# Kernel optimization log

Measured on AMD Instinct MI355X. Metric: run time of the kernel, lower is better.

## Reference

```python
import jax, jax.numpy as jnp
import numpy as np

T, B, I, H = 100, 64, 256, 512


def setup_inputs() -> dict:
    key = jax.random.key(0)
    ks = jax.random.split(key, 7)
    # torch kaiming_uniform_(a=sqrt(5)) + fan_in bias init -> uniform(-1/sqrt(fan_in), 1/sqrt(fan_in))
    b_ih = 1.0 / np.sqrt(I)
    b_hh = 1.0 / np.sqrt(H)
    return {
        "input": jax.random.normal(ks[0], (T, B, I), jnp.float32),
        "initial_h": jax.random.normal(ks[1], (B, H), jnp.float32),
        "initial_c": jax.random.normal(ks[2], (B, H), jnp.float32),
        "weight_ih": jax.random.uniform(ks[3], (4 * H, I), jnp.float32, -b_ih, b_ih),
        "weight_hh": jax.random.uniform(ks[4], (4 * H, H), jnp.float32, -b_hh, b_hh),
        "bias_ih": jax.random.uniform(ks[5], (4 * H,), jnp.float32, -b_ih, b_ih),
        "bias_hh": jax.random.uniform(ks[6], (4 * H,), jnp.float32, -b_hh, b_hh),
    }


def reference(input, initial_h, initial_c, weight_ih, weight_hh, bias_ih, bias_hh):
    Bsz, Isz = input.shape[1], input.shape[2]
    Hs = initial_h.shape[1]

    def step(carry, x_t):
        hx, cx, ev_ih, ev_hh, ev_b = carry
        # standard LSTM gates, torch gate order: i, f, g, o
        gates = x_t @ weight_ih.T + hx @ weight_hh.T + bias_ih + bias_hh  # [B,4H]
        i_g, f_g, g_g, o_g = jnp.split(gates, 4, axis=1)
        i = jax.nn.sigmoid(i_g)
        f = jax.nn.sigmoid(f_g)
        g = jnp.tanh(g_g)
        o = jax.nn.sigmoid(o_g)
        cy = f * cx + i * g
        hy = o * jnp.tanh(cy)
        # e-prop instantaneous derivatives of c_t wrt the i/f/g pre-activations
        d_i = g * i * (1.0 - i)          # [B,H]
        d_f = cx * f * (1.0 - f)
        d_g = i * (1.0 - g * g)
        d = jnp.concatenate([d_i, d_f, d_g], axis=1)[:, :, None]  # [B,3H,1]
        f3 = jnp.tile(f, (1, 3))[:, :, None]                      # [B,3H,1]
        # eligibility-trace recursion: ev_t = f_t * ev_{t-1} + d_t (outer) input
        ev_ih = f3 * ev_ih + d * x_t[:, None, :]   # [B,3H,I]
        ev_hh = f3 * ev_hh + d * hx[:, None, :]    # [B,3H,H]
        ev_b = f3 * ev_b + d                       # [B,3H,1]
        return (hy, cy, ev_ih, ev_hh, ev_b), hy

    ev_ih0 = jnp.zeros((Bsz, 3 * Hs, Isz), input.dtype)
    ev_hh0 = jnp.zeros((Bsz, 3 * Hs, Hs), input.dtype)
    ev_b0 = jnp.zeros((Bsz, 3 * Hs, 1), input.dtype)
    (hx, cx, ev_ih, ev_hh, ev_b), outputs = jax.lax.scan(
        step, (initial_h, initial_c, ev_ih0, ev_hh0, ev_b0), input
    )
    return outputs, cx, ev_ih, ev_hh, ev_b
```

## Files before the change

kernel.cpp:

```cpp
#include <hip/hip_runtime.h>
#include <math.h>

#define TT 100
#define BB 64
#define II 256
#define HH 512
#define G4H 2048
#define G3H 1536
#define NBLK 256

#define OFF_GT    0
#define OFF_HBUF  13107200
#define OFF_FBUF  16416768
#define OFF_DBUF  19693568
#define OFF_CT    29523968
#define OFF_XT    29556736
#define OFF_WIHT  31195136
#define OFF_WHHT  31719424

#define O_OUT   0
#define O_CX    3276800
#define O_EVIH  3309568
#define O_EVHH  28475392
#define O_EVB   78807040

__global__ __launch_bounds__(256) void tp64(const float* __restrict__ src,
                                            float* __restrict__ dst,
                                            int R, int C,
                                            long sstride, long dstride) {
  __shared__ float tile[64][65];
  src += (long)blockIdx.z * sstride;
  dst += (long)blockIdx.z * dstride;
  int r0 = blockIdx.y * 64, c0 = blockIdx.x * 64;
  int tx = threadIdx.x & 15, tq = threadIdx.x >> 4;
#pragma unroll
  for (int p = 0; p < 4; ++p) {
    int rl = p * 16 + tq;
    float4 v = *(const float4*)(src + (long)(r0 + rl) * C + c0 + tx * 4);
    tile[rl][tx * 4 + 0] = v.x; tile[rl][tx * 4 + 1] = v.y;
    tile[rl][tx * 4 + 2] = v.z; tile[rl][tx * 4 + 3] = v.w;
  }
  __syncthreads();
#pragma unroll
  for (int p = 0; p < 4; ++p) {
    int cl = p * 16 + tq;
    float4 v;
    v.x = tile[tx * 4 + 0][cl]; v.y = tile[tx * 4 + 1][cl];
    v.z = tile[tx * 4 + 2][cl]; v.w = tile[tx * 4 + 3][cl];
    *(float4*)(dst + (long)(c0 + cl) * R + r0 + tx * 4) = v;
  }
}

__global__ __launch_bounds__(256) void make_whhg(const float* __restrict__ WhhT,
                                                 float* __restrict__ WhhG,
                                                 int* __restrict__ bar) {
  int gid = blockIdx.x * 256 + threadIdx.x;
  if (gid < NBLK) bar[gid] = 0;
  int k = gid >> 11, j = gid & 2047;
  float v = WhhT[gid];
  WhhG[(long)k * G4H + ((j & 511) << 2) + (j >> 9)] = v;
}

template <int BK, int KTILES, bool BIAS, bool ZSHIFT>
__global__ __launch_bounds__(256) void gemm_tn(
    const float* __restrict__ A, long batchA, int lda,
    const float* __restrict__ Z, long batchZ, int ldz,
    const float* __restrict__ Z0, long batchZ0,
    float* __restrict__ C, long batchC, int ldc,
    const float* __restrict__ bia, const float* __restrict__ bib) {
  __shared__ float As[BK][64];
  __shared__ float Zs[BK][64];
  int tid = threadIdx.x;
  int tn = tid & 15, tm = tid >> 4;
  int m0 = blockIdx.x * 64, n0 = blockIdx.y * 64;
  long bz = blockIdx.z;
  const float* Ab = A + bz * batchA + m0;
  const float* Zb = Z + bz * batchZ + n0;
  const float* Z0b = ZSHIFT ? (Z0 + bz * batchZ0 + n0) : nullptr;
  float acc[4][4] = {};
  for (int kt = 0; kt < KTILES; ++kt) {
    int k0 = kt * BK;
#pragma unroll
    for (int p = tid; p < BK * 64; p += 256) {
      int r = p >> 6, c = p & 63;
      int k = k0 + r;
      As[r][c] = Ab[(long)k * lda + c];
      const float* zr;
      if (ZSHIFT)
        zr = (k == 0) ? Z0b : (Zb + (long)(k - 1) * ldz);
      else
        zr = Zb + (long)k * ldz;
      Zs[r][c] = zr[c];
    }
    __syncthreads();
#pragma unroll 4
    for (int kk = 0; kk < BK; ++kk) {
      float4 a = *(const float4*)&As[kk][tm * 4];
      float4 z = *(const float4*)&Zs[kk][tn * 4];
      float av[4] = {a.x, a.y, a.z, a.w};
      float zv[4] = {z.x, z.y, z.z, z.w};
#pragma unroll
      for (int q = 0; q < 4; ++q)
#pragma unroll
        for (int r = 0; r < 4; ++r)
          acc[q][r] = fmaf(av[q], zv[r], acc[q][r]);
    }
    __syncthreads();
  }
  float* Cb = C + bz * batchC + n0 + tn * 4;
#pragma unroll
  for (int q = 0; q < 4; ++q) {
    int m = m0 + tm * 4 + q;
    float bv = BIAS ? (bia[m] + bib[m]) : 0.f;
    float4 v;
    v.x = acc[q][0] + bv; v.y = acc[q][1] + bv;
    v.z = acc[q][2] + bv; v.w = acc[q][3] + bv;
    *(float4*)(Cb + (long)m * ldc) = v;
  }
}

__global__ __launch_bounds__(512) void lstm_rec(
    const float* __restrict__ G_T, const float* __restrict__ WhhG,
    float* __restrict__ Hbuf, float* __restrict__ cT,
    float* __restrict__ Fbuf, float* __restrict__ Dbuf,
    int* __restrict__ bar) {
  __shared__ float red[8][8][64];
  int tid = threadIdx.x;
  int lane = tid & 63;
  int wave = __builtin_amdgcn_readfirstlane(tid >> 6);
  int bx = blockIdx.x;
  const float* wp = WhhG + (long)(wave * 64) * G4H + bx * 8;
  int h2 = tid >> 6;
  int b = tid & 63;
  float creg = 0.f;
  if (tid < 128) creg = cT[(bx * 2 + h2) * BB + b];

  float gpre0 = 0.f, gpre1 = 0.f, gpre2 = 0.f, gpre3 = 0.f;
  if (tid < 128) {
    const float* gp = G_T + (bx * 2 + h2) * BB + b;
    gpre0 = gp[0l * HH * BB];
    gpre1 = gp[1l * HH * BB];
    gpre2 = gp[2l * HH * BB];
    gpre3 = gp[3l * HH * BB];
  }

  int myflag = wave * 32 + (lane & 31);

  for (int t = 0; t < TT; ++t) {
    const float* hp = Hbuf + (long)t * (HH * BB) + (wave * 64) * BB + lane;
    float hv[64];
#pragma unroll
    for (int k = 0; k < 64; ++k) hv[k] = hp[(long)k * BB];
    float a0 = 0.f, a1 = 0.f, a2 = 0.f, a3 = 0.f;
    float a4 = 0.f, a5 = 0.f, a6 = 0.f, a7 = 0.f;
#pragma unroll
    for (int k = 0; k < 64; ++k) {
      float h = hv[k];
      float4 w0 = *(const float4*)(wp + (long)k * G4H);
      float4 w1 = *(const float4*)(wp + (long)k * G4H + 4);
      a0 = fmaf(w0.x, h, a0); a1 = fmaf(w0.y, h, a1);
      a2 = fmaf(w0.z, h, a2); a3 = fmaf(w0.w, h, a3);
      a4 = fmaf(w1.x, h, a4); a5 = fmaf(w1.y, h, a5);
      a6 = fmaf(w1.z, h, a6); a7 = fmaf(w1.w, h, a7);
    }
    red[wave][0][lane] = a0; red[wave][1][lane] = a1;
    red[wave][2][lane] = a2; red[wave][3][lane] = a3;
    red[wave][4][lane] = a4; red[wave][5][lane] = a5;
    red[wave][6][lane] = a6; red[wave][7][lane] = a7;
    __syncthreads();
    if (tid < 128) {
      float g0 = gpre0, g1 = gpre1, g2 = gpre2, g3 = gpre3;
#pragma unroll
      for (int kp = 0; kp < 8; ++kp) {
        g0 += red[kp][h2 * 4 + 0][b];
        g1 += red[kp][h2 * 4 + 1][b];
        g2 += red[kp][h2 * 4 + 2][b];
        g3 += red[kp][h2 * 4 + 3][b];
      }
      float ig = 1.f / (1.f + expf(-g0));
      float fg = 1.f / (1.f + expf(-g1));
      float gg = tanhf(g2);
      float og = 1.f / (1.f + expf(-g3));
      int idx = (bx * 2 + h2) * BB + b;
      float co = creg;
      float cy = fg * co + ig * gg;
      creg = cy;
      __hip_atomic_store(&Hbuf[(long)(t + 1) * (HH * BB) + idx],
                         og * tanhf(cy), __ATOMIC_RELAXED,
                         __HIP_MEMORY_SCOPE_AGENT);
      Fbuf[(long)t * (HH * BB) + idx] = fg;
      float* dp = Dbuf + (long)t * (G3H * BB) + idx;
      dp[0] = gg * ig * (1.f - ig);
      dp[HH * BB] = co * fg * (1.f - fg);
      dp[2 * HH * BB] = ig * (1.f - gg * gg);
    }
    __syncthreads();
    if (t < TT - 1) {
      if (tid == 0)
        __hip_atomic_store(&bar[bx], t + 1, __ATOMIC_RELAXED,
                           __HIP_MEMORY_SCOPE_AGENT);
      if (tid < 128) {
        const float* gp =
            G_T + (long)(t + 1) * (G4H * BB) + (bx * 2 + h2) * BB + b;
        gpre0 = gp[0l * HH * BB];
        gpre1 = gp[1l * HH * BB];
        gpre2 = gp[2l * HH * BB];
        gpre3 = gp[3l * HH * BB];
      }
      {
        int tgt = t + 1;
        while (true) {
          int v = __hip_atomic_load(&bar[myflag], __ATOMIC_RELAXED,
                                    __HIP_MEMORY_SCOPE_AGENT);
          if (__all(v >= tgt)) break;
          __builtin_amdgcn_s_sleep(1);
        }
      }
      asm volatile("" ::: "memory");
    }
  }
  if (tid < 128) cT[(bx * 2 + h2) * BB + b] = creg;
}

__global__ __launch_bounds__(256) void suffix_scale(float* __restrict__ Dbuf,
                                                    const float* __restrict__ Fbuf,
                                                    float* __restrict__ evb) {
  int g = blockIdx.x * 256 + threadIdx.x;
  int b = g & 63, hh = g >> 6;
  float P = 1.f, e0 = 0.f, e1 = 0.f, e2 = 0.f;
#pragma unroll 2
  for (int t = TT - 1; t >= 0; --t) {
    float* dp = Dbuf + (long)t * (G3H * BB) + hh * BB + b;
    float v0 = dp[0] * P, v1 = dp[HH * BB] * P, v2 = dp[2 * HH * BB] * P;
    dp[0] = v0; dp[HH * BB] = v1; dp[2 * HH * BB] = v2;
    e0 += v0; e1 += v1; e2 += v2;
    P *= Fbuf[(long)t * (HH * BB) + hh * BB + b];
  }
  evb[b * G3H + hh] = e0;
  evb[b * G3H + HH + hh] = e1;
  evb[b * G3H + 2 * HH + hh] = e2;
}

extern "C" void kernel_launch(void* const* d_in, const int* in_sizes, int n_in,
                              void* d_out, int out_size, void* d_ws, size_t ws_size,
                              hipStream_t stream) {
  const float* x   = (const float*)d_in[0];
  const float* h0  = (const float*)d_in[1];
  const float* c0  = (const float*)d_in[2];
  const float* Wih = (const float*)d_in[3];
  const float* Whh = (const float*)d_in[4];
  const float* bih = (const float*)d_in[5];
  const float* bhh = (const float*)d_in[6];
  float* out = (float*)d_out;
  float* ws = (float*)d_ws;

  float* G_T   = ws + OFF_GT;
  float* DbufT = ws + OFF_GT;
  float* Hbuf  = ws + OFF_HBUF;
  float* Fbuf  = ws + OFF_FBUF;
  float* Dbuf  = ws + OFF_DBUF;
  float* cT    = ws + OFF_CT;
  float* xT    = ws + OFF_XT;
  float* WhhG  = ws + OFF_XT;
  float* WihT  = ws + OFF_WIHT;
  int*   bar   = (int*)(ws + OFF_WIHT);
  float* WhhT  = ws + OFF_WHHT;

  tp64<<<dim3(II / 64, G4H / 64, 1), 256, 0, stream>>>(Wih, WihT, G4H, II, 0, 0);
  tp64<<<dim3(HH / 64, G4H / 64, 1), 256, 0, stream>>>(Whh, WhhT, G4H, HH, 0, 0);
  tp64<<<dim3(II / 64, 1, TT), 256, 0, stream>>>(x, xT, BB, II, BB * II, BB * II);
  tp64<<<dim3(HH / 64, 1, 1), 256, 0, stream>>>(h0, Hbuf, BB, HH, 0, 0);
  tp64<<<dim3(HH / 64, 1, 1), 256, 0, stream>>>(c0, cT, BB, HH, 0, 0);

  gemm_tn<64, 4, true, false><<<dim3(G4H / 64, 1, TT), 256, 0, stream>>>(
      WihT, 0, G4H, xT, (long)II * BB, BB, nullptr, 0,
      G_T, (long)G4H * BB, BB, bih, bhh);

  make_whhg<<<dim3(HH * G4H / 256, 1, 1), 256, 0, stream>>>(WhhT, WhhG, bar);

  {
    const float* a_gt = G_T;
    const float* a_wg = WhhG;
    float* a_hb = Hbuf;
    float* a_ct = cT;
    float* a_fb = Fbuf;
    float* a_db = Dbuf;
    int* a_bar = bar;
    void* args[] = {(void*)&a_gt, (void*)&a_wg, (void*)&a_hb, (void*)&a_ct,
                    (void*)&a_fb, (void*)&a_db, (void*)&a_bar};
    hipLaunchCooperativeKernel((const void*)lstm_rec, dim3(NBLK), dim3(512),
                               args, 0, stream);
  }

  suffix_scale<<<dim3(HH * BB / 256, 1, 1), 256, 0, stream>>>(Dbuf, Fbuf,
                                                              out + O_EVB);

  tp64<<<dim3(1, TT * G3H / 64, 1), 256, 0, stream>>>(Dbuf, DbufT, TT * G3H, BB,
                                                      0, 0);

  tp64<<<dim3(1, HH / 64, TT), 256, 0, stream>>>(Hbuf + HH * BB, out + O_OUT,
                                                 HH, BB, HH * BB, HH * BB);
  tp64<<<dim3(1, HH / 64, 1), 256, 0, stream>>>(cT, out + O_CX, HH, BB, 0, 0);

  gemm_tn<20, 5, false, false><<<dim3(G3H / 64, II / 64, BB), 256, 0, stream>>>(
      DbufT, (long)TT * G3H, G3H, x, (long)II, (long)BB * II, nullptr, 0,
      out + O_EVIH, (long)G3H * II, II, nullptr, nullptr);

  gemm_tn<20, 5, false, true><<<dim3(G3H / 64, HH / 64, BB), 256, 0, stream>>>(
      DbufT, (long)TT * G3H, G3H, out + O_OUT, (long)HH, (long)BB * HH,
      h0, (long)HH,
      out + O_EVHH, (long)G3H * HH, HH, nullptr, nullptr);
}
```

Before: 1.568 ms.

## Cache recurrent weights in LDS and pipeline gate waves with per-column flags

Each block of the recurrent LSTM kernel now loads its slice of the recurrent weight matrix into LDS once, instead of re-reading it from global memory every timestep. The block grows to ten waves: eight compute the matvec and two dedicated waves apply the gate nonlinearities one step behind, using a double-buffered reduction array. The single per-block barrier flag is replaced by per-column-pair flags, published after a waitcnt by the gate waves. Consumers spin only on the flags they need, which shortens the global synchronization critical path at the cost of more flag polling and larger blocks.

```diff
diff --git a/kernel.cpp b/kernel.cpp
--- a/kernel.cpp
+++ b/kernel.cpp
@@ -55,7 +55,7 @@
                                                  float* __restrict__ WhhG,
                                                  int* __restrict__ bar) {
   int gid = blockIdx.x * 256 + threadIdx.x;
-  if (gid < NBLK) bar[gid] = 0;
+  if (gid < 2 * NBLK) bar[gid] = 0;
   int k = gid >> 11, j = gid & 2047;
   float v = WhhT[gid];
   WhhG[(long)k * G4H + ((j & 511) << 2) + (j >> 9)] = v;
@@ -119,63 +119,84 @@
   }
 }
 
-__global__ __launch_bounds__(512) void lstm_rec(
+__global__ __launch_bounds__(640) void lstm_rec(
     const float* __restrict__ G_T, const float* __restrict__ WhhG,
     float* __restrict__ Hbuf, float* __restrict__ cT,
     float* __restrict__ Fbuf, float* __restrict__ Dbuf,
     int* __restrict__ bar) {
-  __shared__ float red[8][8][64];
+  __shared__ float lds_w[4096];
+  __shared__ float red[2][8][8][64];
   int tid = threadIdx.x;
   int lane = tid & 63;
   int wave = __builtin_amdgcn_readfirstlane(tid >> 6);
   int bx = blockIdx.x;
-  const float* wp = WhhG + (long)(wave * 64) * G4H + bx * 8;
-  int h2 = tid >> 6;
-  int b = tid & 63;
+
+  {
+    float4* d4 = (float4*)lds_w;
+    const float4* s4 = (const float4*)WhhG;
+    for (int n = tid; n < 1024; n += 640) {
+      int k = n >> 1, half = n & 1;
+      d4[n] = s4[(long)k * 512 + bx * 2 + half];
+    }
+  }
+
+  int h2 = wave - 8;
+  int b = lane;
   float creg = 0.f;
-  if (tid < 128) creg = cT[(bx * 2 + h2) * BB + b];
-
   float gpre0 = 0.f, gpre1 = 0.f, gpre2 = 0.f, gpre3 = 0.f;
-  if (tid < 128) {
+  if (wave >= 8) {
+    creg = cT[(bx * 2 + h2) * BB + b];
     const float* gp = G_T + (bx * 2 + h2) * BB + b;
     gpre0 = gp[0l * HH * BB];
     gpre1 = gp[1l * HH * BB];
     gpre2 = gp[2l * HH * BB];
     gpre3 = gp[3l * HH * BB];
   }
-
-  int myflag = wave * 32 + (lane & 31);
+  __syncthreads();
 
   for (int t = 0; t < TT; ++t) {
-    const float* hp = Hbuf + (long)t * (HH * BB) + (wave * 64) * BB + lane;
-    float hv[64];
-#pragma unroll
-    for (int k = 0; k < 64; ++k) hv[k] = hp[(long)k * BB];
-    float a0 = 0.f, a1 = 0.f, a2 = 0.f, a3 = 0.f;
-    float a4 = 0.f, a5 = 0.f, a6 = 0.f, a7 = 0.f;
-#pragma unroll
-    for (int k = 0; k < 64; ++k) {
-      float h = hv[k];
-      float4 w0 = *(const float4*)(wp + (long)k * G4H);
-      float4 w1 = *(const float4*)(wp + (long)k * G4H + 4);
-      a0 = fmaf(w0.x, h, a0); a1 = fmaf(w0.y, h, a1);
-      a2 = fmaf(w0.z, h, a2); a3 = fmaf(w0.w, h, a3);
-      a4 = fmaf(w1.x, h, a4); a5 = fmaf(w1.y, h, a5);
-      a6 = fmaf(w1.z, h, a6); a7 = fmaf(w1.w, h, a7);
-    }
-    red[wave][0][lane] = a0; red[wave][1][lane] = a1;
-    red[wave][2][lane] = a2; red[wave][3][lane] = a3;
-    red[wave][4][lane] = a4; red[wave][5][lane] = a5;
-    red[wave][6][lane] = a6; red[wave][7][lane] = a7;
-    __syncthreads();
-    if (tid < 128) {
+    if (wave < 8) {
+      if (t > 0) {
+        int myflag = wave * 64 + lane;
+        while (true) {
+          int v = __hip_atomic_load(&bar[myflag], __ATOMIC_RELAXED,
+                                    __HIP_MEMORY_SCOPE_AGENT);
+          if (__all(v >= t)) break;
+          __builtin_amdgcn_s_sleep(1);
+        }
+        asm volatile("" ::: "memory");
+      }
+      const float* hp = Hbuf + (long)t * (HH * BB) + (wave * 64) * BB + lane;
+      float hv[64];
+#pragma unroll
+      for (int k = 0; k < 64; ++k) hv[k] = hp[(long)k * BB];
+      float a0 = 0.f, a1 = 0.f, a2 = 0.f, a3 = 0.f;
+      float a4 = 0.f, a5 = 0.f, a6 = 0.f, a7 = 0.f;
+      const float4* w4 = (const float4*)lds_w + wave * 128;
+#pragma unroll
+      for (int k = 0; k < 64; ++k) {
+        float4 w0 = w4[2 * k];
+        float4 w1 = w4[2 * k + 1];
+        float h = hv[k];
+        a0 = fmaf(w0.x, h, a0); a1 = fmaf(w0.y, h, a1);
+        a2 = fmaf(w0.z, h, a2); a3 = fmaf(w0.w, h, a3);
+        a4 = fmaf(w1.x, h, a4); a5 = fmaf(w1.y, h, a5);
+        a6 = fmaf(w1.z, h, a6); a7 = fmaf(w1.w, h, a7);
+      }
+      int p = t & 1;
+      red[p][wave][0][lane] = a0; red[p][wave][1][lane] = a1;
+      red[p][wave][2][lane] = a2; red[p][wave][3][lane] = a3;
+      red[p][wave][4][lane] = a4; red[p][wave][5][lane] = a5;
+      red[p][wave][6][lane] = a6; red[p][wave][7][lane] = a7;
+    } else if (t > 0) {
+      int p = (t - 1) & 1;
       float g0 = gpre0, g1 = gpre1, g2 = gpre2, g3 = gpre3;
 #pragma unroll
       for (int kp = 0; kp < 8; ++kp) {
-        g0 += red[kp][h2 * 4 + 0][b];
-        g1 += red[kp][h2 * 4 + 1][b];
-        g2 += red[kp][h2 * 4 + 2][b];
-        g3 += red[kp][h2 * 4 + 3][b];
+        g0 += red[p][kp][h2 * 4 + 0][b];
+        g1 += red[p][kp][h2 * 4 + 1][b];
+        g2 += red[p][kp][h2 * 4 + 2][b];
+        g3 += red[p][kp][h2 * 4 + 3][b];
       }
       float ig = 1.f / (1.f + expf(-g0));
       float fg = 1.f / (1.f + expf(-g1));
@@ -185,41 +206,51 @@
       float co = creg;
       float cy = fg * co + ig * gg;
       creg = cy;
-      __hip_atomic_store(&Hbuf[(long)(t + 1) * (HH * BB) + idx],
-                         og * tanhf(cy), __ATOMIC_RELAXED,
-                         __HIP_MEMORY_SCOPE_AGENT);
-      Fbuf[(long)t * (HH * BB) + idx] = fg;
-      float* dp = Dbuf + (long)t * (G3H * BB) + idx;
+      __hip_atomic_store(&Hbuf[(long)t * (HH * BB) + idx], og * tanhf(cy),
+                         __ATOMIC_RELAXED, __HIP_MEMORY_SCOPE_AGENT);
+      Fbuf[(long)(t - 1) * (HH * BB) + idx] = fg;
+      float* dp = Dbuf + (long)(t - 1) * (G3H * BB) + idx;
       dp[0] = gg * ig * (1.f - ig);
       dp[HH * BB] = co * fg * (1.f - fg);
       dp[2 * HH * BB] = ig * (1.f - gg * gg);
+      asm volatile("s_waitcnt vmcnt(0)" ::: "memory");
+      if (lane == 0)
+        __hip_atomic_store(&bar[bx * 2 + h2], t, __ATOMIC_RELAXED,
+                           __HIP_MEMORY_SCOPE_AGENT);
+      const float* gp = G_T + (long)t * (G4H * BB) + (bx * 2 + h2) * BB + b;
+      gpre0 = gp[0l * HH * BB];
+      gpre1 = gp[1l * HH * BB];
+      gpre2 = gp[2l * HH * BB];
+      gpre3 = gp[3l * HH * BB];
     }
     __syncthreads();
-    if (t < TT - 1) {
-      if (tid == 0)
-        __hip_atomic_store(&bar[bx], t + 1, __ATOMIC_RELAXED,
-                           __HIP_MEMORY_SCOPE_AGENT);
-      if (tid < 128) {
-        const float* gp =
-            G_T + (long)(t + 1) * (G4H * BB) + (bx * 2 + h2) * BB + b;
-        gpre0 = gp[0l * HH * BB];
-        gpre1 = gp[1l * HH * BB];
-        gpre2 = gp[2l * HH * BB];
-        gpre3 = gp[3l * HH * BB];
-      }
-      {
-        int tgt = t + 1;
-        while (true) {
-          int v = __hip_atomic_load(&bar[myflag], __ATOMIC_RELAXED,
-                                    __HIP_MEMORY_SCOPE_AGENT);
-          if (__all(v >= tgt)) break;
-          __builtin_amdgcn_s_sleep(1);
-        }
-      }
-      asm volatile("" ::: "memory");
-    }
-  }
-  if (tid < 128) cT[(bx * 2 + h2) * BB + b] = creg;
+  }
+
+  if (wave >= 8) {
+    int p = (TT - 1) & 1;
+    float g0 = gpre0, g1 = gpre1, g2 = gpre2, g3 = gpre3;
+#pragma unroll
+    for (int kp = 0; kp < 8; ++kp) {
+      g0 += red[p][kp][h2 * 4 + 0][b];
+      g1 += red[p][kp][h2 * 4 + 1][b];
+      g2 += red[p][kp][h2 * 4 + 2][b];
+      g3 += red[p][kp][h2 * 4 + 3][b];
+    }
+    float ig = 1.f / (1.f + expf(-g0));
+    float fg = 1.f / (1.f + expf(-g1));
+    float gg = tanhf(g2);
+    float og = 1.f / (1.f + expf(-g3));
+    int idx = (bx * 2 + h2) * BB + b;
+    float co = creg;
+    float cy = fg * co + ig * gg;
+    Hbuf[(long)TT * (HH * BB) + idx] = og * tanhf(cy);
+    Fbuf[(long)(TT - 1) * (HH * BB) + idx] = fg;
+    float* dp = Dbuf + (long)(TT - 1) * (G3H * BB) + idx;
+    dp[0] = gg * ig * (1.f - ig);
+    dp[HH * BB] = co * fg * (1.f - fg);
+    dp[2 * HH * BB] = ig * (1.f - gg * gg);
+    cT[idx] = cy;
+  }
 }
 
 __global__ __launch_bounds__(256) void suffix_scale(float* __restrict__ Dbuf,
@@ -288,7 +319,7 @@
     int* a_bar = bar;
     void* args[] = {(void*)&a_gt, (void*)&a_wg, (void*)&a_hb, (void*)&a_ct,
                     (void*)&a_fb, (void*)&a_db, (void*)&a_bar};
-    hipLaunchCooperativeKernel((const void*)lstm_rec, dim3(NBLK), dim3(512),
+    hipLaunchCooperativeKernel((const void*)lstm_rec, dim3(NBLK), dim3(640),
                                args, 0, stream);
   }
 
```

Result: faster. 1.496 ms (-4.6%).
